# Kernel optimization log

Measured on AMD Instinct MI355X. Metric: run time of the kernel, lower is better.

The kernel has to match this reference:

```python
import jax, jax.numpy as jnp
import numpy as np

B, H, S, D = 4, 16, 1024, 64

def setup_inputs() -> dict:
    key = jax.random.key(0)
    kq, kk, kv, kb, km = jax.random.split(key, 5)
    return {
        "q": jax.random.normal(kq, (B, H, S, D), dtype=jnp.float32),
        "k": jax.random.normal(kk, (B, H, S, D), dtype=jnp.float32),
        "v": jax.random.normal(kv, (B, H, S, D), dtype=jnp.float32),
        "add_attn": jax.random.normal(kb, (B, 1, S, S), dtype=jnp.float32),
        "mask": jax.random.randint(km, (B, 1, 1, S), 0, 2, dtype=jnp.int32),
    }

def reference(q, k, v, add_attn, mask):
    d_emb = q.shape[-1]
    scale = 1.0 / jnp.sqrt(jnp.float32(d_emb)).astype(q.dtype)
    # scores: [B,H,Sq,Sk]
    attn = jnp.einsum('bhqd,bhkd->bhqk', q * scale, k)
    attn = attn + add_attn
    attn = jnp.where(mask == 0, jnp.asarray(-1e9, attn.dtype), attn)
    attn = jax.nn.softmax(attn, axis=-1)  # dropout with p=0 is identity
    output = jnp.einsum('bhqk,bhkd->bhqd', attn, v)
    return (output, attn)
```

## Files before the change

### kernel.cpp

```cpp
#include <hip/hip_runtime.h>
#include <math.h>

#define BB 4
#define HH 16
#define SS 1024
#define DD 64
#define QT 16
#define NKW 4
#define KPW 256

typedef __attribute__((ext_vector_type(8))) short bf16x8;
typedef __attribute__((ext_vector_type(4))) float f32x4;

static __device__ inline unsigned short f2bf(float f) {
    unsigned int u = __float_as_uint(f);
    u += 0x7fff + ((u >> 16) & 1);
    return (unsigned short)(u >> 16);
}

__global__ __launch_bounds__(256) void convert_qk(const float* __restrict__ q,
                                                  const float* __restrict__ k,
                                                  unsigned short* __restrict__ qb,
                                                  unsigned short* __restrict__ kb) {
    const int idx = blockIdx.x * 256 + threadIdx.x;
    float4 qv = ((const float4*)q)[idx];
    float4 kv = ((const float4*)k)[idx];
    ushort4 qo = make_ushort4(f2bf(qv.x), f2bf(qv.y), f2bf(qv.z), f2bf(qv.w));
    ushort4 ko = make_ushort4(f2bf(kv.x), f2bf(kv.y), f2bf(kv.z), f2bf(kv.w));
    ((ushort4*)qb)[idx] = qo;
    ((ushort4*)kb)[idx] = ko;
}

__global__ __launch_bounds__(256) void transpose_v(const float* __restrict__ v,
                                                   unsigned short* __restrict__ vt) {
    const int idx = blockIdx.x * 256 + threadIdx.x;
    const int k  = (idx & 255) * 4;
    const int d  = (idx >> 8) & 63;
    const int bh = idx >> 14;
    const float* vb = v + (size_t)bh * SS * DD;
    ushort4 o = make_ushort4(f2bf(vb[(size_t)(k + 0) * DD + d]),
                             f2bf(vb[(size_t)(k + 1) * DD + d]),
                             f2bf(vb[(size_t)(k + 2) * DD + d]),
                             f2bf(vb[(size_t)(k + 3) * DD + d]));
    ((ushort4*)vt)[idx] = o;
}

__global__ __launch_bounds__(256) void attn_mfma(
    const unsigned short* __restrict__ qb,
    const unsigned short* __restrict__ kb,
    const unsigned short* __restrict__ vtb,
    const float* __restrict__ add_attn,
    const int*   __restrict__ mask,
    float* __restrict__ out,
    float* __restrict__ attn_out)
{
    const int qt = blockIdx.x, h = blockIdx.y, b = blockIdx.z;
    const int bh = b * HH + h;
    const int tid = threadIdx.x;
    const int wave = tid >> 6;
    const int lane = tid & 63;
    const int col  = lane & 15;
    const int quad = lane >> 4;

    __shared__ unsigned short p_tile[NKW][QT][KPW + 8];
    __shared__ float red_m[NKW][QT];
    __shared__ float red_l[NKW][QT];
    __shared__ float o_part[NKW][QT][DD];

    const int q0  = qt * QT;
    const int wk0 = wave * KPW;

    const unsigned short* qrow = qb + ((size_t)bh * SS + q0 + col) * DD + quad * 8;
    const bf16x8 aq0 = *(const bf16x8*)(qrow);
    const bf16x8 aq1 = *(const bf16x8*)(qrow + 32);

    const unsigned short* kbb = kb + (size_t)bh * SS * DD;
    const float* bias = add_attn + ((size_t)b * SS + q0) * SS;
    const int*   mrow = mask + b * SS;

    float s[16][4];
#pragma unroll
    for (int t = 0; t < 16; ++t) {
        const int k0 = wk0 + t * 16;
        const unsigned short* kr = kbb + (size_t)(k0 + col) * DD + quad * 8;
        bf16x8 bk0 = *(const bf16x8*)(kr);
        bf16x8 bk1 = *(const bf16x8*)(kr + 32);
        f32x4 acc = {0.f, 0.f, 0.f, 0.f};
        acc = __builtin_amdgcn_mfma_f32_16x16x32_bf16(aq0, bk0, acc, 0, 0, 0);
        acc = __builtin_amdgcn_mfma_f32_16x16x32_bf16(aq1, bk1, acc, 0, 0, 0);
        const int kidx = k0 + col;
        const int mv = mrow[kidx];
#pragma unroll
        for (int r = 0; r < 4; ++r) {
            const int qr = quad * 4 + r;
            float sv = acc[r] * 0.125f + bias[(size_t)qr * SS + kidx];
            s[t][r] = (mv == 0) ? -1e9f : sv;
        }
    }

    float mx[4];
#pragma unroll
    for (int r = 0; r < 4; ++r) {
        float m = s[0][r];
#pragma unroll
        for (int t = 1; t < 16; ++t) m = fmaxf(m, s[t][r]);
        m = fmaxf(m, __shfl_xor(m, 1));
        m = fmaxf(m, __shfl_xor(m, 2));
        m = fmaxf(m, __shfl_xor(m, 4));
        m = fmaxf(m, __shfl_xor(m, 8));
        mx[r] = m;
    }
    if (col == 0) {
#pragma unroll
        for (int r = 0; r < 4; ++r) red_m[wave][quad * 4 + r] = mx[r];
    }
    __syncthreads();
    float mf[4];
#pragma unroll
    for (int r = 0; r < 4; ++r) {
        const int qr = quad * 4 + r;
        mf[r] = fmaxf(fmaxf(red_m[0][qr], red_m[1][qr]),
                      fmaxf(red_m[2][qr], red_m[3][qr]));
    }

    float ls[4] = {0.f, 0.f, 0.f, 0.f};
#pragma unroll
    for (int t = 0; t < 16; ++t) {
#pragma unroll
        for (int r = 0; r < 4; ++r) {
            float e = __expf(s[t][r] - mf[r]);
            s[t][r] = e;
            ls[r] += e;
        }
    }
#pragma unroll
    for (int r = 0; r < 4; ++r) {
        float l = ls[r];
        l += __shfl_xor(l, 1);
        l += __shfl_xor(l, 2);
        l += __shfl_xor(l, 4);
        l += __shfl_xor(l, 8);
        ls[r] = l;
    }
    if (col == 0) {
#pragma unroll
        for (int r = 0; r < 4; ++r) red_l[wave][quad * 4 + r] = ls[r];
    }
    __syncthreads();
    float inv[4];
#pragma unroll
    for (int r = 0; r < 4; ++r) {
        const int qr = quad * 4 + r;
        inv[r] = 1.0f / (red_l[0][qr] + red_l[1][qr] + red_l[2][qr] + red_l[3][qr]);
    }

    float* arow = attn_out + ((size_t)bh * SS + q0) * SS;
#pragma unroll
    for (int t = 0; t < 16; ++t) {
#pragma unroll
        for (int r = 0; r < 4; ++r) {
            const int qr = quad * 4 + r;
            float p = s[t][r] * inv[r];
            arow[(size_t)qr * SS + wk0 + t * 16 + col] = p;
            p_tile[wave][qr][t * 16 + col] = f2bf(p);
        }
    }

    const unsigned short* vt = vtb + (size_t)bh * DD * SS;
    f32x4 oacc[4];
#pragma unroll
    for (int dc = 0; dc < 4; ++dc) oacc[dc] = (f32x4){0.f, 0.f, 0.f, 0.f};
#pragma unroll
    for (int c = 0; c < 8; ++c) {
        bf16x8 ap = *(const bf16x8*)(&p_tile[wave][col][c * 32 + quad * 8]);
#pragma unroll
        for (int dc = 0; dc < 4; ++dc) {
            const unsigned short* vr =
                vt + (size_t)(dc * 16 + col) * SS + wk0 + c * 32 + quad * 8;
            bf16x8 bv = *(const bf16x8*)(vr);
            oacc[dc] = __builtin_amdgcn_mfma_f32_16x16x32_bf16(ap, bv, oacc[dc], 0, 0, 0);
        }
    }
#pragma unroll
    for (int dc = 0; dc < 4; ++dc)
#pragma unroll
        for (int r = 0; r < 4; ++r)
            o_part[wave][quad * 4 + r][dc * 16 + col] = oacc[dc][r];
    __syncthreads();

    for (int i = tid; i < QT * DD; i += 256) {
        const int qr = i >> 6, d = i & 63;
        out[((size_t)bh * SS + q0 + qr) * DD + d] =
            o_part[0][qr][d] + o_part[1][qr][d] + o_part[2][qr][d] + o_part[3][qr][d];
    }
}

extern "C" void kernel_launch(void* const* d_in, const int* in_sizes, int n_in,
                              void* d_out, int out_size, void* d_ws, size_t ws_size,
                              hipStream_t stream) {
    const float* q        = (const float*)d_in[0];
    const float* k        = (const float*)d_in[1];
    const float* v        = (const float*)d_in[2];
    const float* add_attn = (const float*)d_in[3];
    const int*   mask     = (const int*)d_in[4];

    float* out      = (float*)d_out;
    float* attn_out = (float*)d_out + (size_t)BB * HH * SS * DD;

    const size_t nelem = (size_t)BB * HH * SS * DD;
    unsigned short* qb  = (unsigned short*)d_ws;
    unsigned short* kbb = qb + nelem;
    unsigned short* vtb = kbb + nelem;

    convert_qk<<<dim3(nelem / 4 / 256), dim3(256), 0, stream>>>(q, k, qb, kbb);
    transpose_v<<<dim3(nelem / 4 / 256), dim3(256), 0, stream>>>(v, vtb);

    dim3 grid(SS / QT, HH, BB);
    attn_mfma<<<grid, dim3(256), 0, stream>>>(qb, kbb, vtb, add_attn, mask, out, attn_out);
}
```

Before: 474.6 us.

## Transpose MFMA score layout for vectorized bias/mask loads and coalesced attn stores

Swaps the MFMA operands so each lane owns one query row and four consecutive keys. Bias and mask can then be read as float4/int4, and the softmax reductions become a cross-quad shuffle. The attention matrix is staged as bf16 in shared memory and written back as coalesced float4 rows. The output-partial buffer reuses that same tile, and a launch-bounds occupancy hint is added. The V transpose now goes through a shared-memory tile, so both its reads and writes are coalesced. In exchange, the float32 attention output now carries bf16-rounded probabilities, which reduces its precision.

```diff
diff --git a/kernel.cpp b/kernel.cpp
--- a/kernel.cpp
+++ b/kernel.cpp
@@ -16,6 +16,9 @@
     unsigned int u = __float_as_uint(f);
     u += 0x7fff + ((u >> 16) & 1);
     return (unsigned short)(u >> 16);
+}
+static __device__ inline float bf2f(unsigned short h) {
+    return __uint_as_float(((unsigned int)h) << 16);
 }
 
 __global__ __launch_bounds__(256) void convert_qk(const float* __restrict__ q,
@@ -33,19 +36,33 @@
 
 __global__ __launch_bounds__(256) void transpose_v(const float* __restrict__ v,
                                                    unsigned short* __restrict__ vt) {
-    const int idx = blockIdx.x * 256 + threadIdx.x;
-    const int k  = (idx & 255) * 4;
-    const int d  = (idx >> 8) & 63;
-    const int bh = idx >> 14;
-    const float* vb = v + (size_t)bh * SS * DD;
-    ushort4 o = make_ushort4(f2bf(vb[(size_t)(k + 0) * DD + d]),
-                             f2bf(vb[(size_t)(k + 1) * DD + d]),
-                             f2bf(vb[(size_t)(k + 2) * DD + d]),
-                             f2bf(vb[(size_t)(k + 3) * DD + d]));
-    ((ushort4*)vt)[idx] = o;
-}
-
-__global__ __launch_bounds__(256) void attn_mfma(
+    __shared__ float tile[64][68];
+    const int kt = blockIdx.x, bh = blockIdx.y;
+    const int k0 = kt * 64;
+    const int tid = threadIdx.x;
+    const float* vb = v + ((size_t)bh * SS + k0) * DD;
+
+    const int r  = tid >> 4;
+    const int c4 = (tid & 15) * 4;
+#pragma unroll
+    for (int i = 0; i < 4; ++i) {
+        const int row = i * 16 + r;
+        float4 x = *(const float4*)(vb + (size_t)row * DD + c4);
+        *(float4*)&tile[row][c4] = x;
+    }
+    __syncthreads();
+#pragma unroll
+    for (int i = 0; i < 4; ++i) {
+        const int o  = i * 256 + tid;
+        const int d  = o >> 4;
+        const int kc = (o & 15) * 4;
+        ushort4 y = make_ushort4(f2bf(tile[kc + 0][d]), f2bf(tile[kc + 1][d]),
+                                 f2bf(tile[kc + 2][d]), f2bf(tile[kc + 3][d]));
+        *(ushort4*)(vt + ((size_t)bh * DD + d) * SS + k0 + kc) = y;
+    }
+}
+
+__global__ __launch_bounds__(256, 4) void attn_mfma(
     const unsigned short* __restrict__ qb,
     const unsigned short* __restrict__ kb,
     const unsigned short* __restrict__ vtb,
@@ -62,20 +79,19 @@
     const int col  = lane & 15;
     const int quad = lane >> 4;
 
-    __shared__ unsigned short p_tile[NKW][QT][KPW + 8];
+    __shared__ __align__(16) unsigned short p_tile[NKW][QT][KPW + 8];
     __shared__ float red_m[NKW][QT];
     __shared__ float red_l[NKW][QT];
-    __shared__ float o_part[NKW][QT][DD];
 
     const int q0  = qt * QT;
     const int wk0 = wave * KPW;
 
     const unsigned short* qrow = qb + ((size_t)bh * SS + q0 + col) * DD + quad * 8;
-    const bf16x8 aq0 = *(const bf16x8*)(qrow);
-    const bf16x8 aq1 = *(const bf16x8*)(qrow + 32);
+    const bf16x8 bq0 = *(const bf16x8*)(qrow);
+    const bf16x8 bq1 = *(const bf16x8*)(qrow + 32);
 
     const unsigned short* kbb = kb + (size_t)bh * SS * DD;
-    const float* bias = add_attn + ((size_t)b * SS + q0) * SS;
+    const float* bias = add_attn + ((size_t)b * SS + q0 + col) * SS;
     const int*   mrow = mask + b * SS;
 
     float s[16][4];
@@ -83,88 +99,55 @@
     for (int t = 0; t < 16; ++t) {
         const int k0 = wk0 + t * 16;
         const unsigned short* kr = kbb + (size_t)(k0 + col) * DD + quad * 8;
-        bf16x8 bk0 = *(const bf16x8*)(kr);
-        bf16x8 bk1 = *(const bf16x8*)(kr + 32);
+        bf16x8 ak0 = *(const bf16x8*)(kr);
+        bf16x8 ak1 = *(const bf16x8*)(kr + 32);
         f32x4 acc = {0.f, 0.f, 0.f, 0.f};
-        acc = __builtin_amdgcn_mfma_f32_16x16x32_bf16(aq0, bk0, acc, 0, 0, 0);
-        acc = __builtin_amdgcn_mfma_f32_16x16x32_bf16(aq1, bk1, acc, 0, 0, 0);
-        const int kidx = k0 + col;
-        const int mv = mrow[kidx];
+        acc = __builtin_amdgcn_mfma_f32_16x16x32_bf16(ak0, bq0, acc, 0, 0, 0);
+        acc = __builtin_amdgcn_mfma_f32_16x16x32_bf16(ak1, bq1, acc, 0, 0, 0);
+        const int kbase = k0 + quad * 4;
+        const float4 b4 = *(const float4*)(bias + kbase);
+        const int4   m4 = *(const int4*)(mrow + kbase);
+        s[t][0] = (m4.x == 0) ? -1e9f : acc[0] * 0.125f + b4.x;
+        s[t][1] = (m4.y == 0) ? -1e9f : acc[1] * 0.125f + b4.y;
+        s[t][2] = (m4.z == 0) ? -1e9f : acc[2] * 0.125f + b4.z;
+        s[t][3] = (m4.w == 0) ? -1e9f : acc[3] * 0.125f + b4.w;
+    }
+
+    float mx = s[0][0];
+#pragma unroll
+    for (int t = 0; t < 16; ++t)
+#pragma unroll
+        for (int r = 0; r < 4; ++r) mx = fmaxf(mx, s[t][r]);
+    mx = fmaxf(mx, __shfl_xor(mx, 16));
+    mx = fmaxf(mx, __shfl_xor(mx, 32));
+    if (quad == 0) red_m[wave][col] = mx;
+    __syncthreads();
+    mx = fmaxf(fmaxf(red_m[0][col], red_m[1][col]),
+               fmaxf(red_m[2][col], red_m[3][col]));
+
+    float ls = 0.f;
+#pragma unroll
+    for (int t = 0; t < 16; ++t)
 #pragma unroll
         for (int r = 0; r < 4; ++r) {
-            const int qr = quad * 4 + r;
-            float sv = acc[r] * 0.125f + bias[(size_t)qr * SS + kidx];
-            s[t][r] = (mv == 0) ? -1e9f : sv;
+            float e = __expf(s[t][r] - mx);
+            s[t][r] = e;
+            ls += e;
         }
-    }
-
-    float mx[4];
-#pragma unroll
-    for (int r = 0; r < 4; ++r) {
-        float m = s[0][r];
-#pragma unroll
-        for (int t = 1; t < 16; ++t) m = fmaxf(m, s[t][r]);
-        m = fmaxf(m, __shfl_xor(m, 1));
-        m = fmaxf(m, __shfl_xor(m, 2));
-        m = fmaxf(m, __shfl_xor(m, 4));
-        m = fmaxf(m, __shfl_xor(m, 8));
-        mx[r] = m;
-    }
-    if (col == 0) {
-#pragma unroll
-        for (int r = 0; r < 4; ++r) red_m[wave][quad * 4 + r] = mx[r];
-    }
-    __syncthreads();
-    float mf[4];
-#pragma unroll
-    for (int r = 0; r < 4; ++r) {
-        const int qr = quad * 4 + r;
-        mf[r] = fmaxf(fmaxf(red_m[0][qr], red_m[1][qr]),
-                      fmaxf(red_m[2][qr], red_m[3][qr]));
-    }
-
-    float ls[4] = {0.f, 0.f, 0.f, 0.f};
+    ls += __shfl_xor(ls, 16);
+    ls += __shfl_xor(ls, 32);
+    if (quad == 0) red_l[wave][col] = ls;
+    __syncthreads();
+    const float inv = 1.0f / (red_l[0][col] + red_l[1][col] +
+                              red_l[2][col] + red_l[3][col]);
+
 #pragma unroll
     for (int t = 0; t < 16; ++t) {
-#pragma unroll
-        for (int r = 0; r < 4; ++r) {
-            float e = __expf(s[t][r] - mf[r]);
-            s[t][r] = e;
-            ls[r] += e;
-        }
-    }
-#pragma unroll
-    for (int r = 0; r < 4; ++r) {
-        float l = ls[r];
-        l += __shfl_xor(l, 1);
-        l += __shfl_xor(l, 2);
-        l += __shfl_xor(l, 4);
-        l += __shfl_xor(l, 8);
-        ls[r] = l;
-    }
-    if (col == 0) {
-#pragma unroll
-        for (int r = 0; r < 4; ++r) red_l[wave][quad * 4 + r] = ls[r];
-    }
-    __syncthreads();
-    float inv[4];
-#pragma unroll
-    for (int r = 0; r < 4; ++r) {
-        const int qr = quad * 4 + r;
-        inv[r] = 1.0f / (red_l[0][qr] + red_l[1][qr] + red_l[2][qr] + red_l[3][qr]);
-    }
-
-    float* arow = attn_out + ((size_t)bh * SS + q0) * SS;
-#pragma unroll
-    for (int t = 0; t < 16; ++t) {
-#pragma unroll
-        for (int r = 0; r < 4; ++r) {
-            const int qr = quad * 4 + r;
-            float p = s[t][r] * inv[r];
-            arow[(size_t)qr * SS + wk0 + t * 16 + col] = p;
-            p_tile[wave][qr][t * 16 + col] = f2bf(p);
-        }
-    }
+        ushort4 pk = make_ushort4(f2bf(s[t][0] * inv), f2bf(s[t][1] * inv),
+                                  f2bf(s[t][2] * inv), f2bf(s[t][3] * inv));
+        *(ushort4*)&p_tile[wave][col][t * 16 + quad * 4] = pk;
+    }
+    __syncthreads();
 
     const unsigned short* vt = vtb + (size_t)bh * DD * SS;
     f32x4 oacc[4];
@@ -181,17 +164,42 @@
             oacc[dc] = __builtin_amdgcn_mfma_f32_16x16x32_bf16(ap, bv, oacc[dc], 0, 0, 0);
         }
     }
+
+    float* ab = attn_out + ((size_t)bh * SS + q0) * SS;
+#pragma unroll
+    for (int i = 0; i < 16; ++i) {
+        const int o  = i * 256 + tid;
+        const int qr = o >> 8;
+        const int cc = (o & 255) * 4;
+        const int w  = cc >> 8;
+        const int cl = cc & 255;
+        ushort4 p4 = *(const ushort4*)&p_tile[w][qr][cl];
+        float4 f;
+        f.x = bf2f(p4.x); f.y = bf2f(p4.y); f.z = bf2f(p4.z); f.w = bf2f(p4.w);
+        *(float4*)(ab + (size_t)qr * SS + cc) = f;
+    }
+    __syncthreads();
+
+    float* opw = (float*)&p_tile[wave][0][0];
 #pragma unroll
     for (int dc = 0; dc < 4; ++dc)
 #pragma unroll
         for (int r = 0; r < 4; ++r)
-            o_part[wave][quad * 4 + r][dc * 16 + col] = oacc[dc][r];
-    __syncthreads();
-
-    for (int i = tid; i < QT * DD; i += 256) {
-        const int qr = i >> 6, d = i & 63;
-        out[((size_t)bh * SS + q0 + qr) * DD + d] =
-            o_part[0][qr][d] + o_part[1][qr][d] + o_part[2][qr][d] + o_part[3][qr][d];
+            opw[(quad * 4 + r) * 64 + dc * 16 + col] = oacc[dc][r];
+    __syncthreads();
+
+    {
+        const int qr = tid >> 4, d4 = (tid & 15) * 4;
+        float4 sum;
+        const float* p0 = (const float*)&p_tile[0][0][0] + qr * 64 + d4;
+        const float* p1 = (const float*)&p_tile[1][0][0] + qr * 64 + d4;
+        const float* p2 = (const float*)&p_tile[2][0][0] + qr * 64 + d4;
+        const float* p3 = (const float*)&p_tile[3][0][0] + qr * 64 + d4;
+        sum.x = p0[0] + p1[0] + p2[0] + p3[0];
+        sum.y = p0[1] + p1[1] + p2[1] + p3[1];
+        sum.z = p0[2] + p1[2] + p2[2] + p3[2];
+        sum.w = p0[3] + p1[3] + p2[3] + p3[3];
+        *(float4*)(out + ((size_t)bh * SS + q0 + qr) * DD + d4) = sum;
     }
 }
 
@@ -213,7 +221,7 @@
     unsigned short* vtb = kbb + nelem;
 
     convert_qk<<<dim3(nelem / 4 / 256), dim3(256), 0, stream>>>(q, k, qb, kbb);
-    transpose_v<<<dim3(nelem / 4 / 256), dim3(256), 0, stream>>>(v, vtb);
+    transpose_v<<<dim3(16, 64), dim3(256), 0, stream>>>(v, vtb);
 
     dim3 grid(SS / QT, HH, BB);
     attn_mfma<<<grid, dim3(256), 0, stream>>>(qb, kbb, vtb, add_attn, mask, out, attn_out);
```

New measurement: 480.9 us. Within noise of the previous version (+1.3%).
